# Kernel tuning notes

Measured on AMD Instinct MI355X. Metric: run time of the kernel, lower is better.

Reference implementation:

```python
import jax, jax.numpy as jnp
import numpy as np

N_NODES = 100000

def _gcn_conv(x, W, b, src, dst, n_nodes):
    # PyG GCNConv: h = x @ W; add self-loops; deg over dst; norm = d^-1/2[src]*d^-1/2[dst];
    # out = scatter_add(norm * h[src] -> dst) + b
    h = x @ W  # [N, out]
    deg = jax.ops.segment_sum(jnp.ones_like(dst, dtype=x.dtype), dst, num_segments=n_nodes)
    dinv = jnp.where(deg > 0, jax.lax.rsqrt(deg), 0.0)
    norm = dinv[src] * dinv[dst]  # [E]
    msg = h[src] * norm[:, None]  # [E, out]
    out = jax.ops.segment_sum(msg, dst, num_segments=n_nodes)
    return out + b

def setup_inputs() -> dict:
    key = jax.random.key(0)
    k1, k2, k3, k4 = jax.random.split(key, 4)
    x = jax.random.normal(k1, (N_NODES, 165), dtype=jnp.float32)
    edge_index = jax.random.randint(k2, (2, 1600000), 0, N_NODES, dtype=jnp.int64)
    # glorot-ish init for weights
    W1 = jax.random.normal(k3, (165, 128), dtype=jnp.float32) * (1.0 / np.sqrt(165))
    b1 = jnp.zeros((128,), dtype=jnp.float32)
    W4 = jax.random.normal(k4, (128, 1), dtype=jnp.float32) * (1.0 / np.sqrt(128))
    b4 = jnp.zeros((1,), dtype=jnp.float32)
    return {"x": x, "edge_index": edge_index, "W1": W1, "b1": b1, "W4": W4, "b4": b4}

def reference(x, edge_index, W1, b1, W4, b4):
    n = x.shape[0]
    loop = jnp.arange(n, dtype=edge_index.dtype)
    src = jnp.concatenate([edge_index[0], loop])  # add self-loops
    dst = jnp.concatenate([edge_index[1], loop])
    h = _gcn_conv(x, W1, b1, src, dst, n)
    h = jax.nn.relu(h)
    # dropout p=0.1 is identity at inference (training=False)
    out = _gcn_conv(h, W4, b4, src, dst, n)
    return jax.nn.sigmoid(out)
```

## Files before the change

### kernel.cpp

```cpp
#include <hip/hip_runtime.h>
#include <math.h>

#define N_NODES 100000

using bf16x8 = __attribute__((ext_vector_type(8))) short;
using f32x4  = __attribute__((ext_vector_type(4))) float;

static inline size_t align_up(size_t x, size_t a){ return (x + a - 1) & ~(a - 1); }

__device__ __forceinline__ unsigned short f2bf(float f){
  unsigned u = __float_as_uint(f);
  u = (u + 0x7fffu + ((u >> 16) & 1u)) >> 16;
  return (unsigned short)u;
}
__device__ __forceinline__ float bf2f(unsigned short h){
  return __uint_as_float(((unsigned)h) << 16);
}
__device__ __forceinline__ float bf_lo(unsigned u){ return __uint_as_float(u << 16); }
__device__ __forceinline__ float bf_hi(unsigned u){ return __uint_as_float(u & 0xffff0000u); }

__global__ void k_zero(int* __restrict__ p, int n){
  int i = blockIdx.x*blockDim.x + threadIdx.x;
  if(i < n) p[i] = 0;
}

__global__ void k_convert_count(const int* __restrict__ ei,
                                int* __restrict__ src32, int* __restrict__ dst32,
                                int* __restrict__ rank, int* __restrict__ cnt_p, int E){
  __shared__ int s_is64;
  if(threadIdx.x == 0){
    int is64 = 1;
    for(int k=0;k<64;k++){ if(ei[2*k+1] != 0){ is64 = 0; break; } }
    s_is64 = is64;
  }
  __syncthreads();
  int is64 = s_is64;
  int stride = gridDim.x * blockDim.x;
  for(int e = blockIdx.x*blockDim.x + threadIdx.x; e < E; e += stride){
    int s, d;
    if(is64){ s = ei[2*e]; d = ei[2*(E + e)]; }
    else    { s = ei[e];   d = ei[E + e]; }
    src32[e] = s; dst32[e] = d;
    rank[e] = atomicAdd(&cnt_p[(size_t)d*16], 1);
  }
}

__global__ void k_scan_part(const int* __restrict__ cnt_p, int* __restrict__ bsum, int n){
  __shared__ int red[256];
  int b = blockIdx.x, t = threadIdx.x;
  int base = b*1024 + t*4;
  int s = 0;
  #pragma unroll
  for(int k=0;k<4;k++){ int i = base + k; if(i < n) s += cnt_p[(size_t)i*16]; }
  red[t] = s; __syncthreads();
  for(int off=128; off>0; off>>=1){
    if(t < off) red[t] += red[t+off];
    __syncthreads();
  }
  if(t==0) bsum[b] = red[0];
}

__global__ void k_scan_top(int* __restrict__ bsum, int nb){
  __shared__ int sh[128];
  int t = threadIdx.x;
  int v = (t < nb) ? bsum[t] : 0;
  sh[t] = v; __syncthreads();
  int inc = v;
  for(int off=1; off<128; off<<=1){
    int add = (t >= off) ? sh[t-off] : 0;
    __syncthreads();
    inc += add; sh[t] = inc;
    __syncthreads();
  }
  if(t < nb) bsum[t] = inc - v;
}

__global__ void k_scan_down(const int* __restrict__ cnt_p, const int* __restrict__ bsum,
                            int* __restrict__ offs, float* __restrict__ dinv, int n, int E){
  __shared__ int sh[256];
  int b = blockIdx.x, t = threadIdx.x;
  int base = b*1024 + t*4;
  int c[4]; int local = 0;
  #pragma unroll
  for(int k=0;k<4;k++){ int i = base + k; c[k] = (i < n) ? cnt_p[(size_t)i*16] : 0; local += c[k]; }
  sh[t] = local; __syncthreads();
  int inc = local;
  for(int off=1; off<256; off<<=1){
    int add = (t >= off) ? sh[t-off] : 0;
    __syncthreads();
    inc += add; sh[t] = inc;
    __syncthreads();
  }
  int running = bsum[b] + (inc - local);
  #pragma unroll
  for(int k=0;k<4;k++){
    int i = base + k;
    if(i < n){
      offs[i] = running;
      dinv[i] = rsqrtf((float)(c[k] + 1));
      running += c[k];
    }
  }
  if(b==0 && t==0) offs[n] = E;
}

__global__ void k_fill(const int* __restrict__ src32, const int* __restrict__ dst32,
                       const int* __restrict__ rank, const int* __restrict__ offs,
                       int* __restrict__ csr, int E){
  int stride = gridDim.x * blockDim.x;
  for(int e = blockIdx.x*blockDim.x + threadIdx.x; e < E; e += stride){
    csr[offs[dst32[e]] + rank[e]] = src32[e];
  }
}

__global__ void k_prep_w1(const float* __restrict__ w1, unsigned short* __restrict__ w1b){
  int id = blockIdx.x*blockDim.x + threadIdx.x;
  if(id >= 6*8*64) return;
  int lane = id & 63;
  int st = id >> 6;
  int s = st >> 3, t = st & 7;
  int g = lane >> 4;
  int nn = t*16 + (lane & 15);
  unsigned short* dst = w1b + (size_t)((s*8 + t)*64 + lane)*16;
  #pragma unroll
  for(int j=0;j<8;j++){
    int k = s*32 + g*8 + j;
    float v = (k < 165) ? w1[(size_t)k*128 + nn] : 0.f;
    unsigned short hi = f2bf(v);
    unsigned short lo = f2bf(v - bf2f(hi));
    dst[j] = hi; dst[8+j] = lo;
  }
}

__global__ __launch_bounds__(256) void k_gemm_mfma(const float* __restrict__ x,
                                                   const unsigned short* __restrict__ w1b,
                                                   const float* __restrict__ dinv,
                                                   unsigned short* __restrict__ hsc, int n){
  __shared__ float xs[64*172];
  int t = threadIdx.x;
  int rowbase = blockIdx.x*64;
  int nrow = min(64, n - rowbase);
  int nfl = nrow * 165;
  const float* xblk = x + (size_t)rowbase*165;
  for(int f = t; f < nfl; f += 256){
    int r = f / 165;
    int c = f - r*165;
    xs[r*172 + c] = xblk[f];
  }
  __syncthreads();

  int lane = threadIdx.x & 63;
  int w    = threadIdx.x >> 6;
  int m    = lane & 15;
  int g    = lane >> 4;
  int row  = rowbase + w*16 + m;
  const float* xr = xs + (w*16 + m)*172;
  const bf16x8* wb = (const bf16x8*)w1b;

  f32x4 acc[8];
  #pragma unroll
  for(int q=0;q<8;q++){ acc[q][0]=0.f; acc[q][1]=0.f; acc[q][2]=0.f; acc[q][3]=0.f; }

  #pragma unroll
  for(int s=0;s<6;s++){
    int k0 = s*32 + g*8;
    float v[8];
    if(s < 5){
      #pragma unroll
      for(int j=0;j<8;j++) v[j] = xr[k0+j];
    }else{
      #pragma unroll
      for(int j=0;j<8;j++){ int k = k0+j; v[j] = (k < 165) ? xr[k] : 0.f; }
    }
    bf16x8 ah, al;
    #pragma unroll
    for(int j=0;j<8;j++){
      unsigned short hi = f2bf(v[j]);
      ah[j] = (short)hi;
      al[j] = (short)f2bf(v[j] - bf2f(hi));
    }
    #pragma unroll
    for(int q=0;q<8;q++){
      int bidx = ((s*8 + q)*64 + lane)*2;
      bf16x8 bh = wb[bidx];
      bf16x8 bl = wb[bidx + 1];
      acc[q] = __builtin_amdgcn_mfma_f32_16x16x32_bf16(bh, ah, acc[q], 0, 0, 0);
      acc[q] = __builtin_amdgcn_mfma_f32_16x16x32_bf16(bh, al, acc[q], 0, 0, 0);
      acc[q] = __builtin_amdgcn_mfma_f32_16x16x32_bf16(bl, ah, acc[q], 0, 0, 0);
    }
  }

  if(row < n){
    float di = dinv[row];
    unsigned* hp = (unsigned*)(hsc + (size_t)row*128);
    #pragma unroll
    for(int q=0;q<8;q++){
      unsigned short q0 = f2bf(acc[q][0]*di);
      unsigned short q1 = f2bf(acc[q][1]*di);
      unsigned short q2 = f2bf(acc[q][2]*di);
      unsigned short q3 = f2bf(acc[q][3]*di);
      int nbase = q*16 + g*4;
      hp[(nbase>>1)    ] = (unsigned)q0 | ((unsigned)q1 << 16);
      hp[(nbase>>1) + 1] = (unsigned)q2 | ((unsigned)q3 << 16);
    }
  }
}

__global__ __launch_bounds__(256) void k_agg1(const unsigned short* __restrict__ hsc,
                                              const int* __restrict__ offs,
                                              const int* __restrict__ csr,
                                              const float* __restrict__ dinv,
                                              const float* __restrict__ b1,
                                              const float* __restrict__ w4,
                                              float* __restrict__ g, int n){
  int wv = threadIdx.x >> 6;
  int lane = threadIdx.x & 63;
  int half = lane >> 5;
  int sub  = lane & 31;
  int i = blockIdx.x * 4 + wv;
  if(i >= n) return;

  float di = dinv[i];
  int s0 = offs[i], s1 = offs[i+1];
  const unsigned* base = (const unsigned*)hsc;

  float a0=0.f, a1=0.f, a2=0.f, a3=0.f;
  int e = s0 + half;
  for(; e + 2 < s1; e += 4){
    int sA = csr[e], sB = csr[e+2];
    uint2 uA = *(const uint2*)(base + (size_t)sA*64 + sub*2);
    uint2 uB = *(const uint2*)(base + (size_t)sB*64 + sub*2);
    a0 += bf_lo(uA.x) + bf_lo(uB.x);
    a1 += bf_hi(uA.x) + bf_hi(uB.x);
    a2 += bf_lo(uA.y) + bf_lo(uB.y);
    a3 += bf_hi(uA.y) + bf_hi(uB.y);
  }
  if(e < s1){
    int sA = csr[e];
    uint2 uA = *(const uint2*)(base + (size_t)sA*64 + sub*2);
    a0 += bf_lo(uA.x); a1 += bf_hi(uA.x);
    a2 += bf_lo(uA.y); a3 += bf_hi(uA.y);
  }
  if(half == 0){
    uint2 uS = *(const uint2*)(base + (size_t)i*64 + sub*2);
    a0 += bf_lo(uS.x); a1 += bf_hi(uS.x);
    a2 += bf_lo(uS.y); a3 += bf_hi(uS.y);
  }
  a0 += __shfl_xor(a0, 32, 64);
  a1 += __shfl_xor(a1, 32, 64);
  a2 += __shfl_xor(a2, 32, 64);
  a3 += __shfl_xor(a3, 32, 64);

  int f = sub*4;
  float4 bb  = *(const float4*)&b1[f];
  float4 wv4 = *(const float4*)&w4[f];
  float o0 = fmaxf(di*a0 + bb.x, 0.f);
  float o1 = fmaxf(di*a1 + bb.y, 0.f);
  float o2 = fmaxf(di*a2 + bb.z, 0.f);
  float o3 = fmaxf(di*a3 + bb.w, 0.f);
  float p = o0*wv4.x + o1*wv4.y + o2*wv4.z + o3*wv4.w;
  #pragma unroll
  for(int offm=16; offm>0; offm>>=1) p += __shfl_xor(p, offm, 64);
  if(lane == 0) g[i] = di * p;
}

__global__ void k_agg2c(const float* __restrict__ g, const int* __restrict__ offs,
                        const int* __restrict__ csr, const float* __restrict__ dinv,
                        const float* __restrict__ b4, float* __restrict__ out, int n){
  int lane = threadIdx.x & 63;
  int wv   = threadIdx.x >> 6;
  int sub  = lane & 7;
  int i = blockIdx.x*32 + wv*8 + (lane >> 3);
  if(i >= n) return;
  int s1 = offs[i+1];
  float p = 0.f;
  for(int e = offs[i] + sub; e < s1; e += 8) p += g[csr[e]];
  p += __shfl_xor(p, 4, 8);
  p += __shfl_xor(p, 2, 8);
  p += __shfl_xor(p, 1, 8);
  if(sub == 0){
    float di = dinv[i];
    float z = di*(p + g[i]) + b4[0];
    out[i] = 1.f/(1.f+expf(-z));
  }
}

extern "C" void kernel_launch(void* const* d_in, const int* in_sizes, int n_in,
                              void* d_out, int out_size, void* d_ws, size_t ws_size,
                              hipStream_t stream){
  const float* x  = (const float*)d_in[0];
  const int*   ei = (const int*)d_in[1];
  const float* w1 = (const float*)d_in[2];
  const float* b1 = (const float*)d_in[3];
  const float* w4 = (const float*)d_in[4];
  const float* b4 = (const float*)d_in[5];
  float* out = (float*)d_out;

  const int n = N_NODES;
  const int E = in_sizes[1] / 2;

  char* ws = (char*)d_ws;
  size_t off = 0;
  auto carve = [&](size_t bytes)->void*{
    void* p = ws + off; off = align_up(off + bytes, 256); return p;
  };
  int*   cnt_p = (int*)carve((size_t)n*16*4);
  int*   offs  = (int*)carve((size_t)(n+1)*4);
  int*   bsum  = (int*)carve(128*4);
  float* dinv  = (float*)carve((size_t)n*4);
  int*   src32 = (int*)carve((size_t)E*4);
  int*   dst32 = (int*)carve((size_t)E*4);
  int*   rank  = (int*)carve((size_t)E*4);
  int*   csr   = (int*)carve((size_t)E*4);
  unsigned short* w1b = (unsigned short*)carve((size_t)6*8*64*16*2);
  unsigned short* hsc = (unsigned short*)carve((size_t)n*128*2);
  float* g     = (float*)carve((size_t)n*4);
  (void)ws_size;

  int nb = (n + 1023) / 1024;

  k_zero         <<<(n*16+255)/256, 256, 0, stream>>>(cnt_p, n*16);
  k_convert_count<<<2048, 256, 0, stream>>>(ei, src32, dst32, rank, cnt_p, E);
  k_scan_part    <<<nb, 256, 0, stream>>>(cnt_p, bsum, n);
  k_scan_top     <<<1, 128, 0, stream>>>(bsum, nb);
  k_scan_down    <<<nb, 256, 0, stream>>>(cnt_p, bsum, offs, dinv, n, E);
  k_fill         <<<2048, 256, 0, stream>>>(src32, dst32, rank, offs, csr, E);
  k_prep_w1      <<<12, 256, 0, stream>>>(w1, w1b);
  k_gemm_mfma    <<<(n+63)/64, 256, 0, stream>>>(x, w1b, dinv, hsc, n);
  k_agg1         <<<(n+3)/4, 256, 0, stream>>>(hsc, offs, csr, dinv, b1, w4, g, n);
  k_agg2c        <<<(n+31)/32, 256, 0, stream>>>(g, offs, csr, dinv, b4, out, n);
}
```

Baseline: 350.9 us.

## Privatize degree counters per XCD and widen agg1 gathers to 16 bytes

Degree counting now uses eight per-XCD counter arrays selected by the hardware XCC id, replacing padded global atomics. The rank encodes the local count together with the XCD index. The scan turns the per-XCD counts into per-XCD base offsets, and the fill pass rereads edge_index directly, so the src32 and dst32 intermediates are gone. k_agg1 gathers 16-byte rows, with four edges in flight per wave instead of two. The goal is to cut cross-die atomic contention and memory traffic, at the cost of more scan reads and an edge ordering that is no longer deterministic.

```diff
diff --git a/kernel.cpp b/kernel.cpp
--- a/kernel.cpp
+++ b/kernel.cpp
@@ -19,14 +19,20 @@
 __device__ __forceinline__ float bf_lo(unsigned u){ return __uint_as_float(u << 16); }
 __device__ __forceinline__ float bf_hi(unsigned u){ return __uint_as_float(u & 0xffff0000u); }
 
+__device__ __forceinline__ int xcd_id(){
+  int x;
+  asm volatile("s_getreg_b32 %0, hwreg(HW_REG_XCC_ID)" : "=s"(x));
+  return x & 7;
+}
+
 __global__ void k_zero(int* __restrict__ p, int n){
   int i = blockIdx.x*blockDim.x + threadIdx.x;
   if(i < n) p[i] = 0;
 }
 
 __global__ void k_convert_count(const int* __restrict__ ei,
-                                int* __restrict__ src32, int* __restrict__ dst32,
-                                int* __restrict__ rank, int* __restrict__ cnt_p, int E){
+                                int* __restrict__ rank, int* __restrict__ cnt8,
+                                int E, int n){
   __shared__ int s_is64;
   if(threadIdx.x == 0){
     int is64 = 1;
@@ -35,23 +41,29 @@
   }
   __syncthreads();
   int is64 = s_is64;
+  int r = xcd_id();
+  int* my = cnt8 + (size_t)r * n;
   int stride = gridDim.x * blockDim.x;
   for(int e = blockIdx.x*blockDim.x + threadIdx.x; e < E; e += stride){
-    int s, d;
-    if(is64){ s = ei[2*e]; d = ei[2*(E + e)]; }
-    else    { s = ei[e];   d = ei[E + e]; }
-    src32[e] = s; dst32[e] = d;
-    rank[e] = atomicAdd(&cnt_p[(size_t)d*16], 1);
-  }
-}
-
-__global__ void k_scan_part(const int* __restrict__ cnt_p, int* __restrict__ bsum, int n){
+    int d = is64 ? ei[2*(E + e)] : ei[E + e];
+    int local = atomicAdd(&my[d], 1);
+    rank[e] = (local << 3) | r;
+  }
+}
+
+__global__ void k_scan_part(const int* __restrict__ cnt8, int* __restrict__ bsum, int n){
   __shared__ int red[256];
   int b = blockIdx.x, t = threadIdx.x;
   int base = b*1024 + t*4;
   int s = 0;
   #pragma unroll
-  for(int k=0;k<4;k++){ int i = base + k; if(i < n) s += cnt_p[(size_t)i*16]; }
+  for(int k=0;k<4;k++){
+    int i = base + k;
+    if(i < n){
+      #pragma unroll
+      for(int r=0;r<8;r++) s += cnt8[(size_t)r*n + i];
+    }
+  }
   red[t] = s; __syncthreads();
   for(int off=128; off>0; off>>=1){
     if(t < off) red[t] += red[t+off];
@@ -75,14 +87,21 @@
   if(t < nb) bsum[t] = inc - v;
 }
 
-__global__ void k_scan_down(const int* __restrict__ cnt_p, const int* __restrict__ bsum,
+__global__ void k_scan_down(int* __restrict__ cnt8, const int* __restrict__ bsum,
                             int* __restrict__ offs, float* __restrict__ dinv, int n, int E){
   __shared__ int sh[256];
   int b = blockIdx.x, t = threadIdx.x;
   int base = b*1024 + t*4;
-  int c[4]; int local = 0;
-  #pragma unroll
-  for(int k=0;k<4;k++){ int i = base + k; c[k] = (i < n) ? cnt_p[(size_t)i*16] : 0; local += c[k]; }
+  int tot[4]; int local = 0;
+  #pragma unroll
+  for(int k=0;k<4;k++){
+    int i = base + k; int s = 0;
+    if(i < n){
+      #pragma unroll
+      for(int r=0;r<8;r++) s += cnt8[(size_t)r*n + i];
+    }
+    tot[k] = s; local += s;
+  }
   sh[t] = local; __syncthreads();
   int inc = local;
   for(int off=1; off<256; off<<=1){
@@ -97,19 +116,37 @@
     int i = base + k;
     if(i < n){
       offs[i] = running;
-      dinv[i] = rsqrtf((float)(c[k] + 1));
-      running += c[k];
+      dinv[i] = rsqrtf((float)(tot[k] + 1));
+      int acc = running;
+      #pragma unroll
+      for(int r=0;r<8;r++){
+        int c = cnt8[(size_t)r*n + i];
+        cnt8[(size_t)r*n + i] = acc;
+        acc += c;
+      }
+      running += tot[k];
     }
   }
   if(b==0 && t==0) offs[n] = E;
 }
 
-__global__ void k_fill(const int* __restrict__ src32, const int* __restrict__ dst32,
-                       const int* __restrict__ rank, const int* __restrict__ offs,
-                       int* __restrict__ csr, int E){
+__global__ void k_fill(const int* __restrict__ ei, const int* __restrict__ rank,
+                       const int* __restrict__ cbase, int* __restrict__ csr, int E, int n){
+  __shared__ int s_is64;
+  if(threadIdx.x == 0){
+    int is64 = 1;
+    for(int k=0;k<64;k++){ if(ei[2*k+1] != 0){ is64 = 0; break; } }
+    s_is64 = is64;
+  }
+  __syncthreads();
+  int is64 = s_is64;
   int stride = gridDim.x * blockDim.x;
   for(int e = blockIdx.x*blockDim.x + threadIdx.x; e < E; e += stride){
-    csr[offs[dst32[e]] + rank[e]] = src32[e];
+    int s, d;
+    if(is64){ s = ei[2*e]; d = ei[2*(E + e)]; }
+    else    { s = ei[e];   d = ei[E + e]; }
+    int rk = rank[e];
+    csr[cbase[(size_t)(rk & 7)*n + d] + (rk >> 3)] = s;
   }
 }
 
@@ -215,52 +252,65 @@
                                               float* __restrict__ g, int n){
   int wv = threadIdx.x >> 6;
   int lane = threadIdx.x & 63;
-  int half = lane >> 5;
-  int sub  = lane & 31;
+  int q   = lane >> 4;
+  int sub = lane & 15;
   int i = blockIdx.x * 4 + wv;
   if(i >= n) return;
 
   float di = dinv[i];
   int s0 = offs[i], s1 = offs[i+1];
-  const unsigned* base = (const unsigned*)hsc;
-
-  float a0=0.f, a1=0.f, a2=0.f, a3=0.f;
-  int e = s0 + half;
-  for(; e + 2 < s1; e += 4){
-    int sA = csr[e], sB = csr[e+2];
-    uint2 uA = *(const uint2*)(base + (size_t)sA*64 + sub*2);
-    uint2 uB = *(const uint2*)(base + (size_t)sB*64 + sub*2);
-    a0 += bf_lo(uA.x) + bf_lo(uB.x);
-    a1 += bf_hi(uA.x) + bf_hi(uB.x);
-    a2 += bf_lo(uA.y) + bf_lo(uB.y);
-    a3 += bf_hi(uA.y) + bf_hi(uB.y);
+  const uint4* base = (const uint4*)hsc;
+
+  float a0=0.f,a1=0.f,a2=0.f,a3=0.f,a4=0.f,a5=0.f,a6=0.f,a7=0.f;
+  int e = s0 + q;
+  for(; e + 4 < s1; e += 8){
+    uint4 uA = base[(size_t)csr[e]*16 + sub];
+    uint4 uB = base[(size_t)csr[e+4]*16 + sub];
+    a0 += bf_lo(uA.x) + bf_lo(uB.x);  a1 += bf_hi(uA.x) + bf_hi(uB.x);
+    a2 += bf_lo(uA.y) + bf_lo(uB.y);  a3 += bf_hi(uA.y) + bf_hi(uB.y);
+    a4 += bf_lo(uA.z) + bf_lo(uB.z);  a5 += bf_hi(uA.z) + bf_hi(uB.z);
+    a6 += bf_lo(uA.w) + bf_lo(uB.w);  a7 += bf_hi(uA.w) + bf_hi(uB.w);
   }
   if(e < s1){
-    int sA = csr[e];
-    uint2 uA = *(const uint2*)(base + (size_t)sA*64 + sub*2);
-    a0 += bf_lo(uA.x); a1 += bf_hi(uA.x);
-    a2 += bf_lo(uA.y); a3 += bf_hi(uA.y);
-  }
-  if(half == 0){
-    uint2 uS = *(const uint2*)(base + (size_t)i*64 + sub*2);
-    a0 += bf_lo(uS.x); a1 += bf_hi(uS.x);
-    a2 += bf_lo(uS.y); a3 += bf_hi(uS.y);
-  }
-  a0 += __shfl_xor(a0, 32, 64);
-  a1 += __shfl_xor(a1, 32, 64);
-  a2 += __shfl_xor(a2, 32, 64);
-  a3 += __shfl_xor(a3, 32, 64);
-
-  int f = sub*4;
-  float4 bb  = *(const float4*)&b1[f];
-  float4 wv4 = *(const float4*)&w4[f];
-  float o0 = fmaxf(di*a0 + bb.x, 0.f);
-  float o1 = fmaxf(di*a1 + bb.y, 0.f);
-  float o2 = fmaxf(di*a2 + bb.z, 0.f);
-  float o3 = fmaxf(di*a3 + bb.w, 0.f);
-  float p = o0*wv4.x + o1*wv4.y + o2*wv4.z + o3*wv4.w;
-  #pragma unroll
-  for(int offm=16; offm>0; offm>>=1) p += __shfl_xor(p, offm, 64);
+    uint4 uA = base[(size_t)csr[e]*16 + sub];
+    a0 += bf_lo(uA.x);  a1 += bf_hi(uA.x);
+    a2 += bf_lo(uA.y);  a3 += bf_hi(uA.y);
+    a4 += bf_lo(uA.z);  a5 += bf_hi(uA.z);
+    a6 += bf_lo(uA.w);  a7 += bf_hi(uA.w);
+  }
+  if(q == 0){
+    uint4 uS = base[(size_t)i*16 + sub];
+    a0 += bf_lo(uS.x);  a1 += bf_hi(uS.x);
+    a2 += bf_lo(uS.y);  a3 += bf_hi(uS.y);
+    a4 += bf_lo(uS.z);  a5 += bf_hi(uS.z);
+    a6 += bf_lo(uS.w);  a7 += bf_hi(uS.w);
+  }
+  a0 += __shfl_xor(a0,16,64); a0 += __shfl_xor(a0,32,64);
+  a1 += __shfl_xor(a1,16,64); a1 += __shfl_xor(a1,32,64);
+  a2 += __shfl_xor(a2,16,64); a2 += __shfl_xor(a2,32,64);
+  a3 += __shfl_xor(a3,16,64); a3 += __shfl_xor(a3,32,64);
+  a4 += __shfl_xor(a4,16,64); a4 += __shfl_xor(a4,32,64);
+  a5 += __shfl_xor(a5,16,64); a5 += __shfl_xor(a5,32,64);
+  a6 += __shfl_xor(a6,16,64); a6 += __shfl_xor(a6,32,64);
+  a7 += __shfl_xor(a7,16,64); a7 += __shfl_xor(a7,32,64);
+
+  int f = sub*8;
+  float4 bL = *(const float4*)&b1[f];
+  float4 bH = *(const float4*)&b1[f+4];
+  float4 wL = *(const float4*)&w4[f];
+  float4 wH = *(const float4*)&w4[f+4];
+  float p = fmaxf(di*a0 + bL.x, 0.f)*wL.x
+          + fmaxf(di*a1 + bL.y, 0.f)*wL.y
+          + fmaxf(di*a2 + bL.z, 0.f)*wL.z
+          + fmaxf(di*a3 + bL.w, 0.f)*wL.w
+          + fmaxf(di*a4 + bH.x, 0.f)*wH.x
+          + fmaxf(di*a5 + bH.y, 0.f)*wH.y
+          + fmaxf(di*a6 + bH.z, 0.f)*wH.z
+          + fmaxf(di*a7 + bH.w, 0.f)*wH.w;
+  p += __shfl_xor(p, 1, 64);
+  p += __shfl_xor(p, 2, 64);
+  p += __shfl_xor(p, 4, 64);
+  p += __shfl_xor(p, 8, 64);
   if(lane == 0) g[i] = di * p;
 }
 
@@ -304,27 +354,25 @@
   auto carve = [&](size_t bytes)->void*{
     void* p = ws + off; off = align_up(off + bytes, 256); return p;
   };
-  int*   cnt_p = (int*)carve((size_t)n*16*4);
-  int*   offs  = (int*)carve((size_t)(n+1)*4);
-  int*   bsum  = (int*)carve(128*4);
-  float* dinv  = (float*)carve((size_t)n*4);
-  int*   src32 = (int*)carve((size_t)E*4);
-  int*   dst32 = (int*)carve((size_t)E*4);
-  int*   rank  = (int*)carve((size_t)E*4);
-  int*   csr   = (int*)carve((size_t)E*4);
+  int*   cnt8 = (int*)carve((size_t)8*n*4);
+  int*   offs = (int*)carve((size_t)(n+1)*4);
+  int*   bsum = (int*)carve(128*4);
+  float* dinv = (float*)carve((size_t)n*4);
+  int*   rank = (int*)carve((size_t)E*4);
+  int*   csr  = (int*)carve((size_t)E*4);
   unsigned short* w1b = (unsigned short*)carve((size_t)6*8*64*16*2);
   unsigned short* hsc = (unsigned short*)carve((size_t)n*128*2);
-  float* g     = (float*)carve((size_t)n*4);
+  float* g    = (float*)carve((size_t)n*4);
   (void)ws_size;
 
   int nb = (n + 1023) / 1024;
 
-  k_zero         <<<(n*16+255)/256, 256, 0, stream>>>(cnt_p, n*16);
-  k_convert_count<<<2048, 256, 0, stream>>>(ei, src32, dst32, rank, cnt_p, E);
-  k_scan_part    <<<nb, 256, 0, stream>>>(cnt_p, bsum, n);
+  k_zero         <<<(8*n+255)/256, 256, 0, stream>>>(cnt8, 8*n);
+  k_convert_count<<<2048, 256, 0, stream>>>(ei, rank, cnt8, E, n);
+  k_scan_part    <<<nb, 256, 0, stream>>>(cnt8, bsum, n);
   k_scan_top     <<<1, 128, 0, stream>>>(bsum, nb);
-  k_scan_down    <<<nb, 256, 0, stream>>>(cnt_p, bsum, offs, dinv, n, E);
-  k_fill         <<<2048, 256, 0, stream>>>(src32, dst32, rank, offs, csr, E);
+  k_scan_down    <<<nb, 256, 0, stream>>>(cnt8, bsum, offs, dinv, n, E);
+  k_fill         <<<2048, 256, 0, stream>>>(ei, rank, cnt8, csr, E, n);
   k_prep_w1      <<<12, 256, 0, stream>>>(w1, w1b);
   k_gemm_mfma    <<<(n+63)/64, 256, 0, stream>>>(x, w1b, dinv, hsc, n);
   k_agg1         <<<(n+3)/4, 256, 0, stream>>>(hsc, offs, csr, dinv, b1, w4, g, n);
```

Result: faster. 323.1 us (-7.9%).
